# Kernel optimization log

Measured on AMD Instinct MI355X. Metric: run time of the kernel, lower is better.

The kernel has to match this reference:

```python
import jax
import jax.numpy as jnp
import numpy as np
from jax import lax

IOU_THRESH = 0.5
TOP, LEFT, BOTTOM, RIGHT = 0, 1, 2, 3


def setup_inputs() -> dict:
    key = jax.random.key(0)
    k1, k2, k3, k4, k5 = jax.random.split(key, 5)
    B, N, C = 4, 3000, 21
    # plausible boxes in (top, left, bottom, right) with positive height/width
    tl = jax.random.uniform(k1, (B, N, 2), dtype=jnp.float32) * 800.0
    wh = jax.random.uniform(k2, (B, N, 2), dtype=jnp.float32) * 200.0 + 1.0
    nms_reg = jnp.concatenate([tl, tl + wh], axis=2)
    nms_cls = jax.random.normal(k3, (B, N, 1), dtype=jnp.float32)
    rcnn_reg = jax.random.normal(k4, (B, N, 4), dtype=jnp.float32) * 2.0
    rcnn_cls = jax.random.normal(k5, (B, N, C), dtype=jnp.float32)
    return {"nms_reg": nms_reg, "nms_cls": nms_cls,
            "rcnn_reg": rcnn_reg, "rcnn_cls": rcnn_cls, "reduction": 16}


def _pairwise_iou(boxes):
    # boxes: [N, 4] in (top, left, bottom, right). IoU is invariant to the
    # (x, y) axis permutation the original applies before torchvision.nms.
    t, l, b, r = boxes[:, 0], boxes[:, 1], boxes[:, 2], boxes[:, 3]
    area = jnp.maximum(b - t, 0.0) * jnp.maximum(r - l, 0.0)  # [N]
    ih = jnp.maximum(jnp.minimum(b[:, None], b[None, :]) - jnp.maximum(t[:, None], t[None, :]), 0.0)
    iw = jnp.maximum(jnp.minimum(r[:, None], r[None, :]) - jnp.maximum(l[:, None], l[None, :]), 0.0)
    inter = ih * iw  # [N, N]
    union = area[:, None] + area[None, :] - inter
    return inter / jnp.maximum(union, 1e-9)


def _nms_keep(iou, scores):
    # Greedy NMS over one class. iou: [N, N]; scores: [N] (-inf = not this class).
    # Matches torchvision.ops.nms: suppress boxes with IoU > threshold.
    N = scores.shape[0]
    idx = jnp.arange(N)

    def step(state, _):
        rem, keep = state
        i = jnp.argmax(rem)
        valid = rem[i] > -jnp.inf
        keep = keep.at[i].set(valid)
        suppress = (iou[i] > IOU_THRESH) | (idx == i)
        rem = jnp.where(valid & suppress, -jnp.inf, rem)
        return (rem, keep), None

    (_, keep), _ = lax.scan(step, (scores, jnp.zeros(N, dtype=bool)), None, length=N)
    return keep


def reference(nms_reg, nms_cls, rcnn_reg, rcnn_cls, reduction):
    red = jnp.float32(reduction)
    # round top/left down, bottom/right up on the feature grid, back to pixels
    nms_reg_rounded = jnp.concatenate(
        [jnp.floor(nms_reg[:, :, :2] * red), jnp.ceil(nms_reg[:, :, 2:] * red)],
        axis=2) / red
    # rcnn_reg[:, :, c] += nms_reg_rounded[:, :, c] for all 4 coords
    boxes = rcnn_reg + nms_reg_rounded  # [B, N, 4]
    probs = jax.nn.softmax(rcnn_cls, axis=2)  # [B, N, C]
    nms_cls_sig = jax.nn.sigmoid(nms_cls)

    amax = jnp.argmax(probs, axis=2)  # [B, N]
    C = probs.shape[2]
    class_ids = jnp.arange(1, C)  # skip background class 0
    # per-class masked scores: [B, C-1, N]
    cls_scores = jnp.transpose(probs, (0, 2, 1))[:, 1:, :]
    scores = jnp.where(amax[:, None, :] == class_ids[None, :, None],
                       cls_scores, -jnp.inf)

    iou = jax.vmap(_pairwise_iou)(boxes)  # [B, N, N] (shared across classes)
    keep_per_class = jax.vmap(lambda io, sc: jax.vmap(lambda s: _nms_keep(io, s))(sc))(iou, scores)  # [B, C-1, N]
    keep = jnp.any(keep_per_class, axis=1)  # [B, N]; argmax classes are disjoint

    return (nms_reg_rounded, nms_cls_sig, boxes, probs, keep)
```

## Files before the change

kernel.cpp:

```cpp
#include <hip/hip_runtime.h>
#include <cfloat>
#include <climits>

#define B 4
#define N 3000
#define C 21
#define SORT_N 256
#define WORDS 4
#define NMS_BLOCKS (B * (C - 1))
#define PW_BLOCKS 176
#define PW_ROWS 69
#define TPB 1024
#define PITCH 23


__device__ __forceinline__ int softmax_am(const float* __restrict__ lg,
                                          float* __restrict__ pmax_out,
                                          float* __restrict__ pstore) {
    float m = lg[0];
    #pragma unroll
    for (int c = 1; c < C; ++c) m = fmaxf(m, lg[c]);
    float p[C];
    float sum = 0.0f;
    #pragma unroll
    for (int c = 0; c < C; ++c) {
        p[c] = expf(__fsub_rn(lg[c], m));
        sum = __fadd_rn(sum, p[c]);
    }
    float best = -1.0f; int bc = 0;
    #pragma unroll
    for (int c = 0; c < C; ++c) {
        float pc = __fdiv_rn(p[c], sum);
        if (pstore) pstore[c] = pc;
        if (pc > best) { best = pc; bc = c; }
    }
    *pmax_out = best;
    return bc;
}

__device__ __forceinline__ void make_boxes(float4 nr, float4 rr, float red,
                                           float4* rounded, float4* box) {
    float r0 = floorf(__fmul_rn(nr.x, red)) / red;
    float r1 = floorf(__fmul_rn(nr.y, red)) / red;
    float r2 = ceilf (__fmul_rn(nr.z, red)) / red;
    float r3 = ceilf (__fmul_rn(nr.w, red)) / red;
    *rounded = make_float4(r0, r1, r2, r3);
    *box = make_float4(__fadd_rn(rr.x, r0), __fadd_rn(rr.y, r1),
                       __fadd_rn(rr.z, r2), __fadd_rn(rr.w, r3));
}

__global__ __launch_bounds__(TPB) void fused_kernel(
    const float* __restrict__ nms_reg,
    const float* __restrict__ nms_cls,
    const float* __restrict__ rcnn_reg,
    const float* __restrict__ rcnn_cls,
    const int* __restrict__ red_p,
    float* __restrict__ out)
{
    const int tid = threadIdx.x;

    float* out_round = out;
    float* out_sig   = out + B * N * 4;
    float* out_boxes = out + B * N * 5;
    float* out_probs = out + B * N * 9;
    float* out_keep  = out + B * N * 30;

    if (blockIdx.x >= NMS_BLOCKS) {
        __shared__ float stage[PW_ROWS * PITCH];
        const int pwid = blockIdx.x - NMS_BLOCKS;
        const int row0 = pwid * PW_ROWS;
        const int nrows = min(PW_ROWS, B * N - row0);
        if (nrows <= 0) return;
        const int cnt = nrows * C;

        const float* gl = rcnn_cls + (size_t)row0 * C;
        for (int w = tid; w < cnt; w += TPB) {
            int r = w / C;
            stage[r * PITCH + (w - r * C)] = gl[w];
        }
        __syncthreads();

        if (tid < nrows) {
            const int bn = row0 + tid;
            float red = (float)(*red_p);

            float4 nr = ((const float4*)nms_reg)[bn];
            float4 rr = ((const float4*)rcnn_reg)[bn];
            float4 rounded, box;
            make_boxes(nr, rr, red, &rounded, &box);
            ((float4*)out_round)[bn] = rounded;
            ((float4*)out_boxes)[bn] = box;

            float x = nms_cls[bn];
            float s;
            if (x >= 0.0f) s = 1.0f / (1.0f + expf(-x));
            else { float e = expf(x); s = e / (1.0f + e); }
            out_sig[bn] = s;

            float* row = stage + tid * PITCH;
            float lgv[C];
            #pragma unroll
            for (int cc = 0; cc < C; ++cc) lgv[cc] = row[cc];
            float pm;
            int am = softmax_am(lgv, &pm, row);

            if (am == 0) out_keep[bn] = 0.0f;
        }
        __syncthreads();

        float* po = out_probs + (size_t)row0 * C;
        for (int w = tid; w < cnt; w += TPB) {
            int r = w / C;
            po[w] = stage[r * PITCH + (w - r * C)];
        }
        return;
    }

    const int b = blockIdx.x / (C - 1);
    const int c = blockIdx.x % (C - 1) + 1;
    const int lane = tid & 63;

    __shared__ int   gid[SORT_N];
    __shared__ float gsc[SORT_N];
    __shared__ int   rnk[SORT_N];
    __shared__ int   sid[SORT_N];
    __shared__ float bt[SORT_N], bl[SORT_N], bb[SORT_N], br_[SORT_N], ar[SORT_N];
    __shared__ __align__(16) unsigned long long msk[SORT_N][WORDS];
    __shared__ unsigned long long aout[WORDS];
    __shared__ int mcount;

    if (tid == 0) mcount = 0;
    if (tid < SORT_N) rnk[tid] = 0;
    __syncthreads();

    #pragma unroll
    for (int chunk = 0; chunk < 3; ++chunk) {
        int n = chunk * TPB + tid;
        bool match = false;
        float pm = 0.0f;
        if (n < N) {
            int am = softmax_am(rcnn_cls + (size_t)(b * N + n) * C, &pm, nullptr);
            match = (am == c);
        }
        unsigned long long mb = __ballot(match);
        int base = 0;
        if (lane == 0 && mb) base = atomicAdd(&mcount, __popcll(mb));
        base = __shfl(base, 0);
        if (match) {
            int pos = base + __popcll(mb & ((1ull << lane) - 1ull));
            if (pos < SORT_N) { gid[pos] = n; gsc[pos] = pm; }
        }
    }
    __syncthreads();
    const int M = min(mcount, SORT_N);

    {
        int e = tid & 255, q = tid >> 8;
        if (e < M) {
            float mys = gsc[e]; int myi = gid[e];
            int j0 = q * 64, j1 = min(j0 + 64, M);
            int partial = 0;
            for (int j = j0; j < j1; ++j) {
                float sj = gsc[j]; int ij = gid[j];
                partial += ((sj > mys) || (sj == mys && ij < myi)) ? 1 : 0;
            }
            if (partial) atomicAdd(&rnk[e], partial);
        }
    }
    __syncthreads();

    if (tid < M) {
        float red = (float)(*red_p);
        int n = gid[tid];
        int rank = rnk[tid];
        float4 nr = ((const float4*)nms_reg)[b * N + n];
        float4 rr = ((const float4*)rcnn_reg)[b * N + n];
        float4 rounded, box;
        make_boxes(nr, rr, red, &rounded, &box);
        sid[rank] = n;
        bt[rank] = box.x; bl[rank] = box.y; bb[rank] = box.z; br_[rank] = box.w;
        ar[rank] = __fmul_rn(fmaxf(__fsub_rn(box.z, box.x), 0.0f),
                             fmaxf(__fsub_rn(box.w, box.y), 0.0f));
    }
    __syncthreads();

    {
        int g = tid >> 8;
        int j = tid & 255;
        int w = (tid >> 6) & 3;
        float jt = 0.f, jl = 0.f, jb = 0.f, jr = 0.f, ja = 0.f;
        if (j < M) { jt = bt[j]; jl = bl[j]; jb = bb[j]; jr = br_[j]; ja = ar[j]; }
        int r0 = g * 64, r1 = min(r0 + 64, M);
        const double THR = 0.5 + 0x1p-25;
        for (int r = r0; r < r1; ++r) {
            float rt = bt[r], rl = bl[r], rb = bb[r], rr2 = br_[r], ra = ar[r];
            bool supp = false;
            if (j > r && j < M) {
                float ih = fmaxf(__fsub_rn(fminf(rb, jb), fmaxf(rt, jt)), 0.0f);
                float iw = fmaxf(__fsub_rn(fminf(rr2, jr), fmaxf(rl, jl)), 0.0f);
                float inter = __fmul_rn(ih, iw);
                float uni = __fsub_rn(__fadd_rn(ra, ja), inter);
                float den = fmaxf(uni, 1e-9f);
                supp = ((double)inter > (double)den * THR);
            }
            unsigned long long wm = __ballot(supp);
            if (lane == 0) msk[r][w] = wm;
        }
    }
    __syncthreads();

    if (tid < 64) {
        auto onesk = [](int k) -> unsigned long long {
            return k <= 0 ? 0ull : (k >= 64 ? ~0ull : ((1ull << k) - 1ull));
        };
        unsigned long long a0 = onesk(M), a1 = onesk(M - 64), a2 = onesk(M - 128), a3 = onesk(M - 192);
        {
            int e = min(64, M);
            #pragma unroll 4
            for (int i = 0; i < e; ++i) {
                unsigned long long sel = 0ull - ((a0 >> i) & 1ull);
                a0 &= ~(msk[i][0] & sel);
                a1 &= ~(msk[i][1] & sel);
                a2 &= ~(msk[i][2] & sel);
                a3 &= ~(msk[i][3] & sel);
            }
        }
        {
            int e = min(128, M);
            #pragma unroll 4
            for (int i = 64; i < e; ++i) {
                unsigned long long sel = 0ull - ((a1 >> (i - 64)) & 1ull);
                a1 &= ~(msk[i][1] & sel);
                a2 &= ~(msk[i][2] & sel);
                a3 &= ~(msk[i][3] & sel);
            }
        }
        {
            int e = min(192, M);
            #pragma unroll 4
            for (int i = 128; i < e; ++i) {
                unsigned long long sel = 0ull - ((a2 >> (i - 128)) & 1ull);
                a2 &= ~(msk[i][2] & sel);
                a3 &= ~(msk[i][3] & sel);
            }
        }
        {
            int e = min(256, M);
            #pragma unroll 4
            for (int i = 192; i < e; ++i) {
                unsigned long long sel = 0ull - ((a3 >> (i - 192)) & 1ull);
                a3 &= ~(msk[i][3] & sel);
            }
        }
        if (lane == 0) { aout[0] = a0; aout[1] = a1; aout[2] = a2; aout[3] = a3; }
    }
    __syncthreads();

    if (tid < M) {
        unsigned long long aw = aout[tid >> 6];
        bool kept = (aw >> (tid & 63)) & 1ull;
        int n = sid[tid];
        out_keep[b * N + n] = (kept && n != 0) ? 1.0f : 0.0f;
    }
}

extern "C" void kernel_launch(void* const* d_in, const int* in_sizes, int n_in,
                              void* d_out, int out_size, void* d_ws, size_t ws_size,
                              hipStream_t stream) {
    const float* nms_reg  = (const float*)d_in[0];
    const float* nms_cls  = (const float*)d_in[1];
    const float* rcnn_reg = (const float*)d_in[2];
    const float* rcnn_cls = (const float*)d_in[3];
    const int*   red_p    = (const int*)d_in[4];
    float* out = (float*)d_out;

    dim3 grid(NMS_BLOCKS + PW_BLOCKS);
    fused_kernel<<<grid, TPB, 0, stream>>>(nms_reg, nms_cls, rcnn_reg, rcnn_cls, red_p, out);
}
```

Before: 103.1 us.

## Share per-row argmax and max-prob from pointwise blocks to NMS blocks via flags

Pointwise blocks now write each row's argmax class and max probability into a workspace array and publish a per-block completion flag. NMS blocks spin on those flags and then read the packed words instead of recomputing the 21-way softmax for all rows in every class block. This removes redundant softmax work across the 80 NMS blocks at the cost of inter-block spin synchronisation. The flags are never reset between launches, which risks reading stale data.

```diff
diff --git a/kernel.cpp b/kernel.cpp
--- a/kernel.cpp
+++ b/kernel.cpp
@@ -7,11 +7,12 @@
 #define C 21
 #define SORT_N 256
 #define WORDS 4
+#define PW_BLOCKS 176
 #define NMS_BLOCKS (B * (C - 1))
-#define PW_BLOCKS 176
 #define PW_ROWS 69
 #define TPB 1024
 #define PITCH 23
+#define FLAG_MAGIC 0x5A5A5A5A
 
 
 __device__ __forceinline__ int softmax_am(const float* __restrict__ lg,
@@ -55,7 +56,9 @@
     const float* __restrict__ rcnn_reg,
     const float* __restrict__ rcnn_cls,
     const int* __restrict__ red_p,
-    float* __restrict__ out)
+    float* __restrict__ out,
+    int* __restrict__ flags,
+    unsigned long long* __restrict__ cw)
 {
     const int tid = threadIdx.x;
 
@@ -65,59 +68,70 @@
     float* out_probs = out + B * N * 9;
     float* out_keep  = out + B * N * 30;
 
-    if (blockIdx.x >= NMS_BLOCKS) {
+    if (blockIdx.x < PW_BLOCKS) {
         __shared__ float stage[PW_ROWS * PITCH];
-        const int pwid = blockIdx.x - NMS_BLOCKS;
+        const int pwid = blockIdx.x;
         const int row0 = pwid * PW_ROWS;
         const int nrows = min(PW_ROWS, B * N - row0);
-        if (nrows <= 0) return;
-        const int cnt = nrows * C;
-
-        const float* gl = rcnn_cls + (size_t)row0 * C;
-        for (int w = tid; w < cnt; w += TPB) {
-            int r = w / C;
-            stage[r * PITCH + (w - r * C)] = gl[w];
-        }
+
+        if (nrows > 0) {
+            const int cnt = nrows * C;
+
+            const float* gl = rcnn_cls + (size_t)row0 * C;
+            for (int w = tid; w < cnt; w += TPB) {
+                int r = w / C;
+                stage[r * PITCH + (w - r * C)] = gl[w];
+            }
+            __syncthreads();
+
+            if (tid < nrows) {
+                const int bn = row0 + tid;
+                float red = (float)(*red_p);
+
+                float4 nr = ((const float4*)nms_reg)[bn];
+                float4 rr = ((const float4*)rcnn_reg)[bn];
+                float4 rounded, box;
+                make_boxes(nr, rr, red, &rounded, &box);
+                ((float4*)out_round)[bn] = rounded;
+                ((float4*)out_boxes)[bn] = box;
+
+                float x = nms_cls[bn];
+                float s;
+                if (x >= 0.0f) s = 1.0f / (1.0f + expf(-x));
+                else { float e = expf(x); s = e / (1.0f + e); }
+                out_sig[bn] = s;
+
+                float* row = stage + tid * PITCH;
+                float lgv[C];
+                #pragma unroll
+                for (int cc = 0; cc < C; ++cc) lgv[cc] = row[cc];
+                float pm;
+                int am = softmax_am(lgv, &pm, row);
+
+                cw[bn] = ((unsigned long long)__float_as_uint(pm) << 32) | (unsigned int)am;
+                if (am == 0) out_keep[bn] = 0.0f;
+            }
+            __syncthreads();
+
+            float* po = out_probs + (size_t)row0 * C;
+            for (int w = tid; w < cnt; w += TPB) {
+                int r = w / C;
+                po[w] = stage[r * PITCH + (w - r * C)];
+            }
+        }
+
         __syncthreads();
-
-        if (tid < nrows) {
-            const int bn = row0 + tid;
-            float red = (float)(*red_p);
-
-            float4 nr = ((const float4*)nms_reg)[bn];
-            float4 rr = ((const float4*)rcnn_reg)[bn];
-            float4 rounded, box;
-            make_boxes(nr, rr, red, &rounded, &box);
-            ((float4*)out_round)[bn] = rounded;
-            ((float4*)out_boxes)[bn] = box;
-
-            float x = nms_cls[bn];
-            float s;
-            if (x >= 0.0f) s = 1.0f / (1.0f + expf(-x));
-            else { float e = expf(x); s = e / (1.0f + e); }
-            out_sig[bn] = s;
-
-            float* row = stage + tid * PITCH;
-            float lgv[C];
-            #pragma unroll
-            for (int cc = 0; cc < C; ++cc) lgv[cc] = row[cc];
-            float pm;
-            int am = softmax_am(lgv, &pm, row);
-
-            if (am == 0) out_keep[bn] = 0.0f;
-        }
-        __syncthreads();
-
-        float* po = out_probs + (size_t)row0 * C;
-        for (int w = tid; w < cnt; w += TPB) {
-            int r = w / C;
-            po[w] = stage[r * PITCH + (w - r * C)];
+        if (tid == 0) {
+            __threadfence();
+            __hip_atomic_store(&flags[pwid], FLAG_MAGIC,
+                               __ATOMIC_RELEASE, __HIP_MEMORY_SCOPE_AGENT);
         }
         return;
     }
 
-    const int b = blockIdx.x / (C - 1);
-    const int c = blockIdx.x % (C - 1) + 1;
+    const int nid = blockIdx.x - PW_BLOCKS;
+    const int b = nid / (C - 1);
+    const int cblk = nid % (C - 1) + 1;
     const int lane = tid & 63;
 
     __shared__ int   gid[SORT_N];
@@ -131,6 +145,12 @@
 
     if (tid == 0) mcount = 0;
     if (tid < SORT_N) rnk[tid] = 0;
+
+    if (tid < PW_BLOCKS) {
+        while (__hip_atomic_load(&flags[tid], __ATOMIC_ACQUIRE,
+                                 __HIP_MEMORY_SCOPE_AGENT) != FLAG_MAGIC)
+            __builtin_amdgcn_s_sleep(1);
+    }
     __syncthreads();
 
     #pragma unroll
@@ -139,8 +159,12 @@
         bool match = false;
         float pm = 0.0f;
         if (n < N) {
-            int am = softmax_am(rcnn_cls + (size_t)(b * N + n) * C, &pm, nullptr);
-            match = (am == c);
+            unsigned long long v = __hip_atomic_load(&cw[b * N + n], __ATOMIC_RELAXED,
+                                                     __HIP_MEMORY_SCOPE_AGENT);
+            if ((int)(v & 0xffffffffull) == cblk) {
+                match = true;
+                pm = __uint_as_float((unsigned int)(v >> 32));
+            }
         }
         unsigned long long mb = __ballot(match);
         int base = 0;
@@ -273,7 +297,10 @@
     const float* rcnn_cls = (const float*)d_in[3];
     const int*   red_p    = (const int*)d_in[4];
     float* out = (float*)d_out;
-
-    dim3 grid(NMS_BLOCKS + PW_BLOCKS);
-    fused_kernel<<<grid, TPB, 0, stream>>>(nms_reg, nms_cls, rcnn_reg, rcnn_cls, red_p, out);
+    int* flags = (int*)d_ws;
+    unsigned long long* cw = (unsigned long long*)((char*)d_ws + 1024);
+
+    dim3 grid(PW_BLOCKS + NMS_BLOCKS);
+    fused_kernel<<<grid, TPB, 0, stream>>>(nms_reg, nms_cls, rcnn_reg, rcnn_cls,
+                                           red_p, out, flags, cw);
 }
```

After: 105.6 us. 1.02x slower.
